# Kernel tuning notes

Measured on AMD Instinct MI355X. Metric: run time of the kernel, lower is better.

The kernel has to match this reference:

```python
import jax, jax.numpy as jnp
import numpy as np

BATCH = 1_000_000
IN_DIM = 3
OUT_DIM = 64


def setup_inputs() -> dict:
    key = jax.random.key(0)
    ks = jax.random.split(key, 14)
    names = ["S", "X", "Uz", "Ug", "Ur", "Uh", "Wz", "Wg", "Wr", "Wh", "bz", "bg", "br", "bh"]
    shapes = {
        "S": (BATCH, OUT_DIM), "X": (BATCH, IN_DIM),
        "Uz": (IN_DIM, OUT_DIM), "Ug": (IN_DIM, OUT_DIM), "Ur": (IN_DIM, OUT_DIM), "Uh": (IN_DIM, OUT_DIM),
        "Wz": (OUT_DIM, OUT_DIM), "Wg": (OUT_DIM, OUT_DIM), "Wr": (OUT_DIM, OUT_DIM), "Wh": (OUT_DIM, OUT_DIM),
        "bz": (1, OUT_DIM), "bg": (1, OUT_DIM), "br": (1, OUT_DIM), "bh": (1, OUT_DIM),
    }
    scale = {"S": 1.0, "X": 1.0}
    return {n: (jax.random.normal(k, shapes[n], dtype=jnp.float32) * scale.get(n, 0.2))
            for n, k in zip(names, ks)}


def reference(S, X, Uz, Ug, Ur, Uh, Wz, Wg, Wr, Wh, bz, bg, br, bh):
    # Custom DGM LSTM-style gated layer (activation_1 = activation_2 = tanh).
    Z = jnp.tanh(X @ Uz + S @ Wz + bz)
    G = jnp.tanh(X @ Ug + S @ Wg + bg)
    R = jnp.tanh(X @ Ur + S @ Wr + br)
    H = jnp.tanh(X @ Uh + (S * R) @ Wh + bh)
    S_new = (1.0 - G) * H + Z * S
    return S_new
```

## Files before the change

### kernel.cpp

```cpp
#include <hip/hip_runtime.h>

#define NWT   62500
#define GRID  512
#define WPB   4
#define TOTW  (GRID * WPB)

typedef __attribute__((ext_vector_type(8))) short bf16x8;
typedef __attribute__((ext_vector_type(4))) float f32x4;

static __device__ __forceinline__ short f2b(float f) {
    __bf16 h = (__bf16)f;
    return __builtin_bit_cast(short, h);
}
static __device__ __forceinline__ float b2f(short s) {
    unsigned u = ((unsigned)(unsigned short)s) << 16;
    return __builtin_bit_cast(float, u);
}
static __device__ __forceinline__ unsigned pack2(float lo, float hi) {
    return ((unsigned)(unsigned short)f2b(lo)) |
           (((unsigned)(unsigned short)f2b(hi)) << 16);
}
static __device__ __forceinline__ float tanh_fast(float x) {
    float e = __expf(2.0f * x);
    return 1.0f - 2.0f * __builtin_amdgcn_rcpf(e + 1.0f);
}

static __device__ __forceinline__ void gate_mm(const bf16x8 (&wR)[2][4],
                                               const char* lBg, const int (&baOff)[4],
                                               bf16x8 aX, bf16x8 a0, bf16x8 a1,
                                               f32x4 (&acc)[4])
{
    #pragma unroll
    for (int nt = 0; nt < 4; ++nt) {
        bf16x8 bx = *(const bf16x8*)(lBg + baOff[nt]);
        f32x4 z4 = {0.f, 0.f, 0.f, 0.f};
        acc[nt] = __builtin_amdgcn_mfma_f32_16x16x32_bf16(aX, bx, z4, 0, 0, 0);
    }
    #pragma unroll
    for (int ks = 0; ks < 2; ++ks) {
        bf16x8 a = ks ? a1 : a0;
        #pragma unroll
        for (int nt = 0; nt < 4; ++nt)
            acc[nt] = __builtin_amdgcn_mfma_f32_16x16x32_bf16(a, wR[ks][nt], acc[nt], 0, 0, 0);
    }
}

__global__ __launch_bounds__(256, 2)
void dgm_lstm_kernel(const float* __restrict__ S, const float* __restrict__ X,
                     const float* __restrict__ U0, const float* __restrict__ U1,
                     const float* __restrict__ U2, const float* __restrict__ U3,
                     const float* __restrict__ W0, const float* __restrict__ W1,
                     const float* __restrict__ W2, const float* __restrict__ W3,
                     const float* __restrict__ b0, const float* __restrict__ b1,
                     const float* __restrict__ b2, const float* __restrict__ b3,
                     float* __restrict__ Out)
{
    __shared__ __align__(16) unsigned short lWT[4][64][64];
    __shared__ __align__(16) unsigned short lBa[4][65][8];
    __shared__ __align__(16) float          lS[WPB][16][68];
    __shared__ __align__(16) unsigned short lR[WPB][16][64];

    const int tid = threadIdx.x;

    {
        const float* Ws[4] = {W0, W1, W2, W3};
        #pragma unroll
        for (int g = 0; g < 4; ++g) {
            #pragma unroll
            for (int it = 0; it < 8; ++it) {
                int p  = it * 256 + tid;
                int n  = p & 63;
                int k2 = (p >> 6) << 1;
                float w0 = Ws[g][k2 * 64 + n];
                float w1 = Ws[g][k2 * 64 + 64 + n];
                int byt = ((n << 7) + (k2 << 1)) ^ ((n & 7) << 4);
                *(unsigned*)((char*)(&lWT[0][0][0]) + (g << 13) + byt) = pack2(w0, w1);
            }
        }
        const float* Us[4] = {U0, U1, U2, U3};
        const float* bs[4] = {b0, b1, b2, b3};
        int g = tid >> 6, n = tid & 63;
        bf16x8 f = {};
        f[0] = f2b(Us[g][n]);       f[1] = f2b(Us[g][64 + n]);
        f[2] = f2b(Us[g][128 + n]); f[3] = f2b(bs[g][n]);
        *(bf16x8*)(&lBa[g][n][0]) = f;
        if (tid < 4) { bf16x8 z = {}; *(bf16x8*)(&lBa[tid][64][0]) = z; }
    }
    __syncthreads();

    const int l   = tid & 63;
    const int wv  = tid >> 6;
    const int l15 = l & 15;
    const int lg  = l >> 4;

    const char* lWb = (const char*)(&lWT[0][0][0]);
    const char* lBb = (const char*)(&lBa[0][0][0]);
    char*       lRw = (char*)(&lR[wv][0][0]);

    bf16x8 wReg[4][2][4];
    {
        #pragma unroll
        for (int g = 0; g < 4; ++g)
            #pragma unroll
            for (int ks = 0; ks < 2; ++ks)
                #pragma unroll
                for (int nt = 0; nt < 4; ++nt) {
                    int n = l15 + (nt << 4);
                    int byt = ((n << 7) + (ks << 6) + (lg << 4)) ^ ((n & 7) << 4);
                    wReg[g][ks][nt] = *(const bf16x8*)(lWb + (g << 13) + byt);
                }
    }

    int baOff[4];
    #pragma unroll
    for (int nt = 0; nt < 4; ++nt)
        baOff[nt] = ((lg == 0) ? (l15 + (nt << 4)) : 64) << 4;
    int rdOff[2];
    #pragma unroll
    for (int ks = 0; ks < 2; ++ks)
        rdOff[ks] = ((l15 << 7) + (ks << 6) + (lg << 4)) ^ ((l15 & 7) << 4);

    const int gw = blockIdx.x * WPB + wv;
    const short one_bf = (short)0x3F80;

    float4 p0, p1, p2, p3;
    float  px0 = 0.f, px1 = 0.f, px2 = 0.f;
    {
        const float* Sr = S + (size_t)((gw << 4) + l15) * 64 + (lg << 3);
        p0 = *(const float4*)(Sr);      p1 = *(const float4*)(Sr + 4);
        p2 = *(const float4*)(Sr + 32); p3 = *(const float4*)(Sr + 36);
        if (lg == 0) {
            const float* Xr = X + (size_t)((gw << 4) + l15) * 3;
            px0 = Xr[0]; px1 = Xr[1]; px2 = Xr[2];
        }
    }

    for (int wt = gw; wt < NWT; wt += TOTW) {
        const int row0 = wt << 4;

        float* lSr = &lS[wv][l15][0];
        *(float4*)(lSr + (lg << 3))      = p0;
        *(float4*)(lSr + (lg << 3) + 4)  = p1;
        *(float4*)(lSr + (lg << 3) + 32) = p2;
        *(float4*)(lSr + (lg << 3) + 36) = p3;

        bf16x8 aS0, aS1, aX = {};
        aS0[0] = f2b(p0.x); aS0[1] = f2b(p0.y); aS0[2] = f2b(p0.z); aS0[3] = f2b(p0.w);
        aS0[4] = f2b(p1.x); aS0[5] = f2b(p1.y); aS0[6] = f2b(p1.z); aS0[7] = f2b(p1.w);
        aS1[0] = f2b(p2.x); aS1[1] = f2b(p2.y); aS1[2] = f2b(p2.z); aS1[3] = f2b(p2.w);
        aS1[4] = f2b(p3.x); aS1[5] = f2b(p3.y); aS1[6] = f2b(p3.z); aS1[7] = f2b(p3.w);
        aX[0] = f2b(px0); aX[1] = f2b(px1); aX[2] = f2b(px2);
        aX[3] = (lg == 0) ? one_bf : (short)0;

        int tn = wt + TOTW;
        if (tn < NWT) {
            const float* Sr = S + (size_t)((tn << 4) + l15) * 64 + (lg << 3);
            p0 = *(const float4*)(Sr);      p1 = *(const float4*)(Sr + 4);
            p2 = *(const float4*)(Sr + 32); p3 = *(const float4*)(Sr + 36);
            if (lg == 0) {
                const float* Xr = X + (size_t)((tn << 4) + l15) * 3;
                px0 = Xr[0]; px1 = Xr[1]; px2 = Xr[2];
            }
        }

        asm volatile("s_waitcnt lgkmcnt(0)" ::: "memory");
        float sv[4][4];
        #pragma unroll
        for (int m = 0; m < 4; ++m)
            #pragma unroll
            for (int nt = 0; nt < 4; ++nt)
                sv[m][nt] = lS[wv][(lg << 2) + m][l15 + (nt << 4)];

        f32x4 acc[4];

        gate_mm(wReg[2], lBb + 2 * 1040, baOff, aX, aS0, aS1, acc);
        #pragma unroll
        for (int nt = 0; nt < 4; ++nt) {
            int n = l15 + (nt << 4);
            #pragma unroll
            for (int m = 0; m < 4; ++m) {
                float t  = tanh_fast(acc[nt][m]);
                int rowm = (lg << 2) + m;
                int byt  = ((rowm << 7) + (n << 1)) ^ ((rowm & 7) << 4);
                *(unsigned short*)(lRw + byt) = (unsigned short)f2b(t);
            }
        }

        float zs[4][4];
        gate_mm(wReg[0], lBb, baOff, aX, aS0, aS1, acc);
        #pragma unroll
        for (int nt = 0; nt < 4; ++nt)
            #pragma unroll
            for (int m = 0; m < 4; ++m)
                zs[nt][m] = tanh_fast(acc[nt][m]) * sv[m][nt];

        float gq[4][4];
        gate_mm(wReg[1], lBb + 1040, baOff, aX, aS0, aS1, acc);
        #pragma unroll
        for (int nt = 0; nt < 4; ++nt)
            #pragma unroll
            for (int m = 0; m < 4; ++m)
                gq[nt][m] = 1.0f - tanh_fast(acc[nt][m]);

        asm volatile("s_waitcnt lgkmcnt(0)" ::: "memory");
        bf16x8 aR0 = *(const bf16x8*)(lRw + rdOff[0]);
        bf16x8 aR1 = *(const bf16x8*)(lRw + rdOff[1]);
        bf16x8 aH0, aH1;
        #pragma unroll
        for (int i = 0; i < 8; ++i) {
            aH0[i] = f2b(b2f(aS0[i]) * b2f(aR0[i]));
            aH1[i] = f2b(b2f(aS1[i]) * b2f(aR1[i]));
        }
        gate_mm(wReg[3], lBb + 3 * 1040, baOff, aX, aH0, aH1, acc);

        float* Or = Out + (size_t)(row0 + (lg << 2)) * 64 + l15;
        #pragma unroll
        for (int nt = 0; nt < 4; ++nt) {
            #pragma unroll
            for (int m = 0; m < 4; ++m) {
                float h = tanh_fast(acc[nt][m]);
                Or[m * 64 + (nt << 4)] = fmaf(gq[nt][m], h, zs[nt][m]);
            }
        }
    }
}

extern "C" void kernel_launch(void* const* d_in, const int* in_sizes, int n_in,
                              void* d_out, int out_size, void* d_ws, size_t ws_size,
                              hipStream_t stream) {
    dim3 grid(GRID), block(256);
    dgm_lstm_kernel<<<grid, block, 0, stream>>>(
        (const float*)d_in[0],  (const float*)d_in[1],
        (const float*)d_in[2],  (const float*)d_in[3],
        (const float*)d_in[4],  (const float*)d_in[5],
        (const float*)d_in[6],  (const float*)d_in[7],
        (const float*)d_in[8],  (const float*)d_in[9],
        (const float*)d_in[10], (const float*)d_in[11],
        (const float*)d_in[12], (const float*)d_in[13],
        (float*)d_out);
}
```

Baseline: 132.8 us.

## Stream gate weights from LDS instead of registers and raise waves per block

The per-lane register cache of all four gate weight matrices (32 bf16x8 vectors per lane) is dropped, and B operands are now read from the swizzled LDS copy inside each MFMA loop. Freeing those registers lets the block grow from 4 to 6 waves, with launch bounds raised to 384 threads and 3 blocks per CU. The goal is more resident waves to hide global load latency on this memory-bound kernel. The cost is extra LDS read traffic on every gate, plus more LDS per block (the per-wave S and R buffers grow with WPB), which may cap how many blocks actually fit.

```diff
diff --git a/kernel.cpp b/kernel.cpp
--- a/kernel.cpp
+++ b/kernel.cpp
@@ -2,7 +2,7 @@
 
 #define NWT   62500
 #define GRID  512
-#define WPB   4
+#define WPB   6
 #define TOTW  (GRID * WPB)
 
 typedef __attribute__((ext_vector_type(8))) short bf16x8;
@@ -25,8 +25,8 @@
     return 1.0f - 2.0f * __builtin_amdgcn_rcpf(e + 1.0f);
 }
 
-static __device__ __forceinline__ void gate_mm(const bf16x8 (&wR)[2][4],
-                                               const char* lBg, const int (&baOff)[4],
+static __device__ __forceinline__ void gate_mm(const char* lWg, const char* lBg,
+                                               const int (&baOff)[4], const int (&wOff)[2][4],
                                                bf16x8 aX, bf16x8 a0, bf16x8 a1,
                                                f32x4 (&acc)[4])
 {
@@ -40,12 +40,14 @@
     for (int ks = 0; ks < 2; ++ks) {
         bf16x8 a = ks ? a1 : a0;
         #pragma unroll
-        for (int nt = 0; nt < 4; ++nt)
-            acc[nt] = __builtin_amdgcn_mfma_f32_16x16x32_bf16(a, wR[ks][nt], acc[nt], 0, 0, 0);
-    }
-}
-
-__global__ __launch_bounds__(256, 2)
+        for (int nt = 0; nt < 4; ++nt) {
+            bf16x8 bw = *(const bf16x8*)(lWg + wOff[ks][nt]);
+            acc[nt] = __builtin_amdgcn_mfma_f32_16x16x32_bf16(a, bw, acc[nt], 0, 0, 0);
+        }
+    }
+}
+
+__global__ __launch_bounds__(384, 3)
 void dgm_lstm_kernel(const float* __restrict__ S, const float* __restrict__ X,
                      const float* __restrict__ U0, const float* __restrict__ U1,
                      const float* __restrict__ U2, const float* __restrict__ U3,
@@ -67,24 +69,30 @@
         #pragma unroll
         for (int g = 0; g < 4; ++g) {
             #pragma unroll
-            for (int it = 0; it < 8; ++it) {
-                int p  = it * 256 + tid;
-                int n  = p & 63;
-                int k2 = (p >> 6) << 1;
-                float w0 = Ws[g][k2 * 64 + n];
-                float w1 = Ws[g][k2 * 64 + 64 + n];
-                int byt = ((n << 7) + (k2 << 1)) ^ ((n & 7) << 4);
-                *(unsigned*)((char*)(&lWT[0][0][0]) + (g << 13) + byt) = pack2(w0, w1);
-            }
-        }
-        const float* Us[4] = {U0, U1, U2, U3};
-        const float* bs[4] = {b0, b1, b2, b3};
-        int g = tid >> 6, n = tid & 63;
-        bf16x8 f = {};
-        f[0] = f2b(Us[g][n]);       f[1] = f2b(Us[g][64 + n]);
-        f[2] = f2b(Us[g][128 + n]); f[3] = f2b(bs[g][n]);
-        *(bf16x8*)(&lBa[g][n][0]) = f;
-        if (tid < 4) { bf16x8 z = {}; *(bf16x8*)(&lBa[tid][64][0]) = z; }
+            for (int it = 0; it < 6; ++it) {
+                int p = it * 384 + tid;
+                if (p < 2048) {
+                    int n  = p & 63;
+                    int k2 = (p >> 6) << 1;
+                    float w0 = Ws[g][k2 * 64 + n];
+                    float w1 = Ws[g][k2 * 64 + 64 + n];
+                    int byt = ((n << 7) + (k2 << 1)) ^ ((n & 7) << 4);
+                    *(unsigned*)((char*)(&lWT[0][0][0]) + (g << 13) + byt) = pack2(w0, w1);
+                }
+            }
+        }
+        if (tid < 256) {
+            const float* Us[4] = {U0, U1, U2, U3};
+            const float* bs[4] = {b0, b1, b2, b3};
+            int g = tid >> 6, n = tid & 63;
+            bf16x8 f = {};
+            f[0] = f2b(Us[g][n]);       f[1] = f2b(Us[g][64 + n]);
+            f[2] = f2b(Us[g][128 + n]); f[3] = f2b(bs[g][n]);
+            *(bf16x8*)(&lBa[g][n][0]) = f;
+        } else if (tid < 260) {
+            bf16x8 z = {};
+            *(bf16x8*)(&lBa[tid - 256][64][0]) = z;
+        }
     }
     __syncthreads();
 
@@ -97,24 +105,18 @@
     const char* lBb = (const char*)(&lBa[0][0][0]);
     char*       lRw = (char*)(&lR[wv][0][0]);
 
-    bf16x8 wReg[4][2][4];
-    {
-        #pragma unroll
-        for (int g = 0; g < 4; ++g)
-            #pragma unroll
-            for (int ks = 0; ks < 2; ++ks)
-                #pragma unroll
-                for (int nt = 0; nt < 4; ++nt) {
-                    int n = l15 + (nt << 4);
-                    int byt = ((n << 7) + (ks << 6) + (lg << 4)) ^ ((n & 7) << 4);
-                    wReg[g][ks][nt] = *(const bf16x8*)(lWb + (g << 13) + byt);
-                }
-    }
-
     int baOff[4];
     #pragma unroll
     for (int nt = 0; nt < 4; ++nt)
         baOff[nt] = ((lg == 0) ? (l15 + (nt << 4)) : 64) << 4;
+    int wOff[2][4];
+    #pragma unroll
+    for (int ks = 0; ks < 2; ++ks)
+        #pragma unroll
+        for (int nt = 0; nt < 4; ++nt) {
+            int n = l15 + (nt << 4);
+            wOff[ks][nt] = ((n << 7) + (ks << 6) + (lg << 4)) ^ ((n & 7) << 4);
+        }
     int rdOff[2];
     #pragma unroll
     for (int ks = 0; ks < 2; ++ks)
@@ -173,7 +175,7 @@
 
         f32x4 acc[4];
 
-        gate_mm(wReg[2], lBb + 2 * 1040, baOff, aX, aS0, aS1, acc);
+        gate_mm(lWb + (2 << 13), lBb + 2 * 1040, baOff, wOff, aX, aS0, aS1, acc);
         #pragma unroll
         for (int nt = 0; nt < 4; ++nt) {
             int n = l15 + (nt << 4);
@@ -187,7 +189,7 @@
         }
 
         float zs[4][4];
-        gate_mm(wReg[0], lBb, baOff, aX, aS0, aS1, acc);
+        gate_mm(lWb, lBb, baOff, wOff, aX, aS0, aS1, acc);
         #pragma unroll
         for (int nt = 0; nt < 4; ++nt)
             #pragma unroll
@@ -195,7 +197,7 @@
                 zs[nt][m] = tanh_fast(acc[nt][m]) * sv[m][nt];
 
         float gq[4][4];
-        gate_mm(wReg[1], lBb + 1040, baOff, aX, aS0, aS1, acc);
+        gate_mm(lWb + (1 << 13), lBb + 1040, baOff, wOff, aX, aS0, aS1, acc);
         #pragma unroll
         for (int nt = 0; nt < 4; ++nt)
             #pragma unroll
@@ -211,7 +213,7 @@
             aH0[i] = f2b(b2f(aS0[i]) * b2f(aR0[i]));
             aH1[i] = f2b(b2f(aS1[i]) * b2f(aR1[i]));
         }
-        gate_mm(wReg[3], lBb + 3 * 1040, baOff, aX, aH0, aH1, acc);
+        gate_mm(lWb + (3 << 13), lBb + 3 * 1040, baOff, wOff, aX, aH0, aH1, acc);
 
         float* Or = Out + (size_t)(row0 + (lg << 2)) * 64 + l15;
         #pragma unroll
@@ -228,7 +230,7 @@
 extern "C" void kernel_launch(void* const* d_in, const int* in_sizes, int n_in,
                               void* d_out, int out_size, void* d_ws, size_t ws_size,
                               hipStream_t stream) {
-    dim3 grid(GRID), block(256);
+    dim3 grid(GRID), block(384);
     dgm_lstm_kernel<<<grid, block, 0, stream>>>(
         (const float*)d_in[0],  (const float*)d_in[1],
         (const float*)d_in[2],  (const float*)d_in[3],
```

Result: slower. 147.6 us (+11.1%).

## Transpose MFMA operands so each lane holds contiguous output columns

Applied to the files above, without the earlier changes.

Swaps the A and B operands of every MFMA, so the accumulator holds the transposed tile and each lane owns four consecutive columns of one row. This lets the S tile be read from LDS as f32x4, the output be stored as float4 instead of scalar stores, and S*R be computed in fp32 and written to LDS packed as uint2, replacing scalar bf16 stores and the bf16 multiply loop. The intent is fewer LDS and global store instructions and better store coalescing. The swizzled write offsets have to match the existing read pattern for the S*R operand.

```diff
diff --git a/kernel.cpp b/kernel.cpp
--- a/kernel.cpp
+++ b/kernel.cpp
@@ -11,10 +11,6 @@
 static __device__ __forceinline__ short f2b(float f) {
     __bf16 h = (__bf16)f;
     return __builtin_bit_cast(short, h);
-}
-static __device__ __forceinline__ float b2f(short s) {
-    unsigned u = ((unsigned)(unsigned short)s) << 16;
-    return __builtin_bit_cast(float, u);
 }
 static __device__ __forceinline__ unsigned pack2(float lo, float hi) {
     return ((unsigned)(unsigned short)f2b(lo)) |
@@ -34,14 +30,14 @@
     for (int nt = 0; nt < 4; ++nt) {
         bf16x8 bx = *(const bf16x8*)(lBg + baOff[nt]);
         f32x4 z4 = {0.f, 0.f, 0.f, 0.f};
-        acc[nt] = __builtin_amdgcn_mfma_f32_16x16x32_bf16(aX, bx, z4, 0, 0, 0);
+        acc[nt] = __builtin_amdgcn_mfma_f32_16x16x32_bf16(bx, aX, z4, 0, 0, 0);
     }
     #pragma unroll
     for (int ks = 0; ks < 2; ++ks) {
         bf16x8 a = ks ? a1 : a0;
         #pragma unroll
         for (int nt = 0; nt < 4; ++nt)
-            acc[nt] = __builtin_amdgcn_mfma_f32_16x16x32_bf16(a, wR[ks][nt], acc[nt], 0, 0, 0);
+            acc[nt] = __builtin_amdgcn_mfma_f32_16x16x32_bf16(wR[ks][nt], a, acc[nt], 0, 0, 0);
     }
 }
 
@@ -98,23 +94,25 @@
     char*       lRw = (char*)(&lR[wv][0][0]);
 
     bf16x8 wReg[4][2][4];
-    {
-        #pragma unroll
-        for (int g = 0; g < 4; ++g)
-            #pragma unroll
-            for (int ks = 0; ks < 2; ++ks)
-                #pragma unroll
-                for (int nt = 0; nt < 4; ++nt) {
-                    int n = l15 + (nt << 4);
-                    int byt = ((n << 7) + (ks << 6) + (lg << 4)) ^ ((n & 7) << 4);
-                    wReg[g][ks][nt] = *(const bf16x8*)(lWb + (g << 13) + byt);
-                }
-    }
+    #pragma unroll
+    for (int g = 0; g < 4; ++g)
+        #pragma unroll
+        for (int ks = 0; ks < 2; ++ks)
+            #pragma unroll
+            for (int nt = 0; nt < 4; ++nt) {
+                int n = l15 + (nt << 4);
+                int byt = ((n << 7) + (ks << 6) + (lg << 4)) ^ ((n & 7) << 4);
+                wReg[g][ks][nt] = *(const bf16x8*)(lWb + (g << 13) + byt);
+            }
 
     int baOff[4];
     #pragma unroll
     for (int nt = 0; nt < 4; ++nt)
         baOff[nt] = ((lg == 0) ? (l15 + (nt << 4)) : 64) << 4;
+    int wrOff[4];
+    #pragma unroll
+    for (int nt = 0; nt < 4; ++nt)
+        wrOff[nt] = ((l15 << 7) + (nt << 5) + (lg << 3)) ^ ((l15 & 7) << 4);
     int rdOff[2];
     #pragma unroll
     for (int ks = 0; ks < 2; ++ks)
@@ -164,63 +162,58 @@
         }
 
         asm volatile("s_waitcnt lgkmcnt(0)" ::: "memory");
-        float sv[4][4];
-        #pragma unroll
-        for (int m = 0; m < 4; ++m)
-            #pragma unroll
-            for (int nt = 0; nt < 4; ++nt)
-                sv[m][nt] = lS[wv][(lg << 2) + m][l15 + (nt << 4)];
+        f32x4 sv[4];
+        #pragma unroll
+        for (int nt = 0; nt < 4; ++nt)
+            sv[nt] = *(const f32x4*)(&lS[wv][l15][(nt << 4) + (lg << 2)]);
 
         f32x4 acc[4];
 
         gate_mm(wReg[2], lBb + 2 * 1040, baOff, aX, aS0, aS1, acc);
         #pragma unroll
         for (int nt = 0; nt < 4; ++nt) {
-            int n = l15 + (nt << 4);
-            #pragma unroll
-            for (int m = 0; m < 4; ++m) {
-                float t  = tanh_fast(acc[nt][m]);
-                int rowm = (lg << 2) + m;
-                int byt  = ((rowm << 7) + (n << 1)) ^ ((rowm & 7) << 4);
-                *(unsigned short*)(lRw + byt) = (unsigned short)f2b(t);
-            }
-        }
-
-        float zs[4][4];
+            float sr0 = sv[nt][0] * tanh_fast(acc[nt][0]);
+            float sr1 = sv[nt][1] * tanh_fast(acc[nt][1]);
+            float sr2 = sv[nt][2] * tanh_fast(acc[nt][2]);
+            float sr3 = sv[nt][3] * tanh_fast(acc[nt][3]);
+            uint2 w;
+            w.x = pack2(sr0, sr1);
+            w.y = pack2(sr2, sr3);
+            *(uint2*)(lRw + wrOff[nt]) = w;
+        }
+
+        f32x4 zs;
+        float zsv[4][4];
         gate_mm(wReg[0], lBb, baOff, aX, aS0, aS1, acc);
         #pragma unroll
         for (int nt = 0; nt < 4; ++nt)
             #pragma unroll
-            for (int m = 0; m < 4; ++m)
-                zs[nt][m] = tanh_fast(acc[nt][m]) * sv[m][nt];
+            for (int j = 0; j < 4; ++j)
+                zsv[nt][j] = tanh_fast(acc[nt][j]) * sv[nt][j];
+        (void)zs;
 
         float gq[4][4];
         gate_mm(wReg[1], lBb + 1040, baOff, aX, aS0, aS1, acc);
         #pragma unroll
         for (int nt = 0; nt < 4; ++nt)
             #pragma unroll
-            for (int m = 0; m < 4; ++m)
-                gq[nt][m] = 1.0f - tanh_fast(acc[nt][m]);
+            for (int j = 0; j < 4; ++j)
+                gq[nt][j] = 1.0f - tanh_fast(acc[nt][j]);
 
         asm volatile("s_waitcnt lgkmcnt(0)" ::: "memory");
         bf16x8 aR0 = *(const bf16x8*)(lRw + rdOff[0]);
         bf16x8 aR1 = *(const bf16x8*)(lRw + rdOff[1]);
-        bf16x8 aH0, aH1;
-        #pragma unroll
-        for (int i = 0; i < 8; ++i) {
-            aH0[i] = f2b(b2f(aS0[i]) * b2f(aR0[i]));
-            aH1[i] = f2b(b2f(aS1[i]) * b2f(aR1[i]));
-        }
-        gate_mm(wReg[3], lBb + 3 * 1040, baOff, aX, aH0, aH1, acc);
-
-        float* Or = Out + (size_t)(row0 + (lg << 2)) * 64 + l15;
+        gate_mm(wReg[3], lBb + 3 * 1040, baOff, aX, aR0, aR1, acc);
+
+        float* Or = Out + (size_t)(row0 + l15) * 64 + (lg << 2);
         #pragma unroll
         for (int nt = 0; nt < 4; ++nt) {
-            #pragma unroll
-            for (int m = 0; m < 4; ++m) {
-                float h = tanh_fast(acc[nt][m]);
-                Or[m * 64 + (nt << 4)] = fmaf(gq[nt][m], h, zs[nt][m]);
-            }
+            float4 o;
+            o.x = fmaf(gq[nt][0], tanh_fast(acc[nt][0]), zsv[nt][0]);
+            o.y = fmaf(gq[nt][1], tanh_fast(acc[nt][1]), zsv[nt][1]);
+            o.z = fmaf(gq[nt][2], tanh_fast(acc[nt][2]), zsv[nt][2]);
+            o.w = fmaf(gq[nt][3], tanh_fast(acc[nt][3]), zsv[nt][3]);
+            *(float4*)(Or + (nt << 4)) = o;
         }
     }
 }
```

Result: faster. 121.4 us (-8.6%).
